# Kernel tuning notes

Measured on AMD Instinct MI355X. Metric: run time of the kernel, lower is better.

Reference implementation:

```python
import jax, jax.numpy as jnp
import numpy as np

LAYERS = 5      # lstm_layers
H = 1           # lstm_hidden_size
IN = 21         # 9 (rot) + 6 (v) + 6 (u)
NEG = 0.1       # LeakyReLU negative slope
EPS = 1e-5      # BatchNorm1d eps


def _lstm_cell(x, h, c, w_ih, w_hh):
    # torch gate order: i, f, g, o ; no biases (lstm_bias=False)
    gates = x @ w_ih.T + h @ w_hh.T              # [k, 4H]
    i, f, g, o = jnp.split(gates, 4, axis=-1)
    i = jax.nn.sigmoid(i)
    f = jax.nn.sigmoid(f)
    g = jnp.tanh(g)
    o = jax.nn.sigmoid(o)
    c_new = f * c + i * g
    h_new = o * jnp.tanh(c_new)
    return h_new, c_new


def _bn_train(z, gamma, beta):
    # BatchNorm1d in training mode: batch stats, biased variance
    m = z.mean(axis=0)
    var = z.var(axis=0)
    return gamma * (z - m) / jnp.sqrt(var + EPS) + beta


def setup_inputs() -> dict:
    key = jax.random.key(0)
    ks = jax.random.split(key, 14)
    k, T = 65536, 32
    s = 0.2  # init scale, roughly torch uniform(-1/sqrt(H)) magnitude
    inp = {
        "r": jax.random.normal(ks[0], (k, T, 9), jnp.float32),
        "v": jax.random.normal(ks[1], (k, T, 6), jnp.float32),
        "u": jax.random.normal(ks[2], (k, T, 6), jnp.float32),
        # LSTM weights: layer 0 sees IN features, layers 1..4 see H
        "w_ih0": jax.random.normal(ks[3], (4 * H, IN), jnp.float32) * s,
        "w_ih_rest": jax.random.normal(ks[4], (LAYERS - 1, 4 * H, H), jnp.float32) * s,
        "w_hh": jax.random.normal(ks[5], (LAYERS, 4 * H, H), jnp.float32) * s,
        # FC head: Linear(H,32,no bias) -> BN -> LReLU -> Linear(32,32) -> BN -> LReLU -> Linear(32,6)
        "W1": jax.random.normal(ks[6], (32, H), jnp.float32) * s,
        "g1": jnp.ones((32,), jnp.float32),
        "b1": jnp.zeros((32,), jnp.float32),
        "W2": jax.random.normal(ks[7], (32, 32), jnp.float32) * s,
        "g2": jnp.ones((32,), jnp.float32),
        "b2": jnp.zeros((32,), jnp.float32),
        "W3": jax.random.normal(ks[8], (6, 32), jnp.float32) * s,
    }
    return inp


def reference(r, v, u, w_ih0, w_ih_rest, w_hh, W1, g1, b1, W2, g2, b2, W3):
    x = jnp.concatenate([r, v, u], axis=-1)          # [k, T, 21]
    k = x.shape[0]
    h0 = jnp.zeros((LAYERS, k, H), x.dtype)
    c0 = jnp.zeros((LAYERS, k, H), x.dtype)
    xs = jnp.swapaxes(x, 0, 1)                       # [T, k, 21]

    def step(carry, xt):
        h, c = carry
        hs, cs = [], []
        layer_in = xt
        for l in range(LAYERS):
            w_ih = w_ih0 if l == 0 else w_ih_rest[l - 1]
            hl, cl = _lstm_cell(layer_in, h[l], c[l], w_ih, w_hh[l])
            hs.append(hl)
            cs.append(cl)
            layer_in = hl
        return (jnp.stack(hs), jnp.stack(cs)), layer_in  # top-layer output

    (hT, cT), outs = jax.lax.scan(step, (h0, c0), xs)    # outs: [T, k, H]

    # fc applied to out[:, 0] -> first timestep of top layer
    y = outs[0]                                          # [k, H]
    y = jax.nn.leaky_relu(_bn_train(y @ W1.T, g1, b1), NEG)
    y = jax.nn.leaky_relu(_bn_train(y @ W2.T, g2, b2), NEG)
    dv = y @ W3.T                                        # [k, 6]
    return dv[:, None], hT, cT
```

## Files before the change

### kernel.cpp

```cpp
#include <hip/hip_runtime.h>
#include <hip/hip_fp16.h>
#include <math.h>

#define T 32
#define NEGS 0.1f
#define EPS 1e-5f
#define NREG 33
#define NH (3 * NREG)


__device__ __forceinline__ float rcp_fast(float x) { return __builtin_amdgcn_rcpf(x); }
__device__ __forceinline__ float sigm(float x) { return rcp_fast(1.0f + __expf(-x)); }
__device__ __forceinline__ float tanh_fast(float x) {
    float t = __expf(2.0f * fabsf(x));
    float r = 1.0f - 2.0f * rcp_fast(t + 1.0f);
    return copysignf(r, x);
}
__device__ __forceinline__ float lrelu(float x) { return x > 0.0f ? x : NEGS * x; }

__device__ __forceinline__ void bn1_ab(const float* __restrict__ W1,
                                       const float* __restrict__ g1,
                                       const float* __restrict__ b1,
                                       float my, float vy, int j,
                                       float& a, float& b, float& tau, int& flip)
{
    float wj = W1[j];
    a = g1[j] * wj * rsqrtf(fmaf(wj * wj, vy, EPS));
    b = b1[j];
    if (a > 0.0f)      { tau = my - b / a; flip = 0; }
    else if (a < 0.0f) { tau = my - b / a; flip = 1; }
    else               { tau = (b > 0.0f ? -__builtin_inff() : __builtin_inff()); flip = 0; }
}

__device__ __forceinline__ void reduce_stats(const double* __restrict__ bSums, int nb, int k,
                                             float* outMy, float* outVy)
{
    const int tid = threadIdx.x;
    double sy = 0.0, sq = 0.0;
    for (int i = tid; i < nb; i += 256) { sy += bSums[2 * i]; sq += bSums[2 * i + 1]; }
#pragma unroll
    for (int off = 32; off; off >>= 1) {
        sy += __shfl_down(sy, off);
        sq += __shfl_down(sq, off);
    }
    __shared__ double dS[4], dQ[4];
    const int wid = tid >> 6, lane = tid & 63;
    if (lane == 0) { dS[wid] = sy; dQ[wid] = sq; }
    __syncthreads();
    if (tid == 0) {
        double tS = dS[0] + dS[1] + dS[2] + dS[3];
        double tQ = dQ[0] + dQ[1] + dQ[2] + dQ[3];
        float my = (float)(tS / k);
        *outMy = my;
        *outVy = (float)(tQ / k) - my * my;
    }
    __syncthreads();
}

__global__ __launch_bounds__(256)
void gates_kernel(const float* __restrict__ r, const float* __restrict__ v,
                  const float* __restrict__ u, const float* __restrict__ wih0,
                  ushort4* __restrict__ xg, int k)
{
    __shared__ float inS[4 * 1344];
    __shared__ ushort4 gbuf[8 * 33];
    const int tid = threadIdx.x;
    const int w = tid >> 6, lane = tid & 63;
    const int s0 = blockIdx.x * 8;

    float wi0[4][21];
#pragma unroll
    for (int g = 0; g < 4; ++g)
#pragma unroll
        for (int j = 0; j < 21; ++j) wi0[g][j] = wih0[g * 21 + j];

    {
        const int sw = s0 + 2 * w;
        const float4* rG = (const float4*)(r + (size_t)sw * 288);
        const float4* vG = (const float4*)(v + (size_t)sw * 192);
        const float4* uG = (const float4*)(u + (size_t)sw * 192);
        float4* wS = ((float4*)inS) + w * 336;
#pragma unroll
        for (int it = 0; it < 6; ++it) {
            int i = lane + it * 64;
            if (i < 336) {
                float4 val = (i < 144) ? rG[i] : (i < 240 ? vG[i - 144] : uG[i - 240]);
                wS[i] = val;
            }
        }
    }
    const int sl = (lane >> 5), t = lane & 31;
    const float* base = inS + w * 1344;
    float x[21];
#pragma unroll
    for (int j = 0; j < 9; ++j) x[j] = base[sl * 288 + t * 9 + j];
#pragma unroll
    for (int j = 0; j < 6; ++j) x[9 + j] = base[576 + sl * 192 + t * 6 + j];
#pragma unroll
    for (int j = 0; j < 6; ++j) x[15 + j] = base[960 + sl * 192 + t * 6 + j];

    float acc[4];
#pragma unroll
    for (int g = 0; g < 4; ++g) {
        float a = 0.f;
#pragma unroll
        for (int j = 0; j < 21; ++j) a = fmaf(wi0[g][j], x[j], a);
        acc[g] = a;
    }
    ushort4 pk;
    pk.x = __half_as_ushort(__float2half(acc[0]));
    pk.y = __half_as_ushort(__float2half(acc[1]));
    pk.z = __half_as_ushort(__float2half(acc[2]));
    pk.w = __half_as_ushort(__float2half(acc[3]));

    const int sblk = 2 * w + sl;
    gbuf[sblk * 33 + t] = pk;
    __syncthreads();

    const int tS = tid >> 3, sS = tid & 7;
    xg[(size_t)tS * k + s0 + sS] = gbuf[sS * 33 + tS];
}

__global__ __launch_bounds__(256, 1)
void recur_kernel(const ushort4* __restrict__ xg, const float* __restrict__ wihr,
                  const float* __restrict__ whhp, float* __restrict__ out,
                  double* __restrict__ bSums, float* __restrict__ wsy, int k)
{
    const int s = blockIdx.x * 256 + threadIdx.x;

    float wir[4][4];
#pragma unroll
    for (int l = 0; l < 4; ++l)
#pragma unroll
        for (int g = 0; g < 4; ++g) wir[l][g] = wihr[l * 4 + g];
    float whh[5][4];
#pragma unroll
    for (int l = 0; l < 5; ++l)
#pragma unroll
        for (int g = 0; g < 4; ++g) whh[l][g] = whhp[l * 4 + g];

    ushort4 gbuf[T];
#pragma unroll
    for (int t = 0; t < T; ++t) gbuf[t] = xg[(size_t)t * k + s];

    float h[5] = {0.f, 0.f, 0.f, 0.f, 0.f};
    float c[5] = {0.f, 0.f, 0.f, 0.f, 0.f};
    float y0 = 0.f;

#pragma unroll
    for (int t = 0; t < T; ++t) {
        const ushort4 G = gbuf[t];
        float a0 = fmaf(whh[0][0], h[0], __half2float(__ushort_as_half(G.x)));
        float a1 = fmaf(whh[0][1], h[0], __half2float(__ushort_as_half(G.y)));
        float a2 = fmaf(whh[0][2], h[0], __half2float(__ushort_as_half(G.z)));
        float a3 = fmaf(whh[0][3], h[0], __half2float(__ushort_as_half(G.w)));
        {
            float ii = sigm(a0), ff = sigm(a1);
            float gg = tanh_fast(a2), oo = sigm(a3);
            c[0] = ff * c[0] + ii * gg;
            h[0] = oo * tanh_fast(c[0]);
        }
        float xin = h[0];
#pragma unroll
        for (int l = 1; l < 5; ++l) {
            float b0 = fmaf(wir[l - 1][0], xin, whh[l][0] * h[l]);
            float b1 = fmaf(wir[l - 1][1], xin, whh[l][1] * h[l]);
            float b2 = fmaf(wir[l - 1][2], xin, whh[l][2] * h[l]);
            float b3 = fmaf(wir[l - 1][3], xin, whh[l][3] * h[l]);
            float ii = sigm(b0), ff = sigm(b1);
            float gg = tanh_fast(b2), oo = sigm(b3);
            c[l] = ff * c[l] + ii * gg;
            h[l] = oo * tanh_fast(c[l]);
            xin = h[l];
        }
        if (t == 0) y0 = h[4];
    }

#pragma unroll
    for (int l = 0; l < 5; ++l) {
        out[(size_t)6 * k + (size_t)l * k + s] = h[l];
        out[(size_t)11 * k + (size_t)l * k + s] = c[l];
    }
    wsy[s] = y0;

    float ys = y0, yq = y0 * y0;
#pragma unroll
    for (int off = 32; off; off >>= 1) {
        ys += __shfl_down(ys, off);
        yq += __shfl_down(yq, off);
    }
    __shared__ float pS[4], pQ[4];
    const int wid = threadIdx.x >> 6, lane = threadIdx.x & 63;
    if (lane == 0) { pS[wid] = ys; pQ[wid] = yq; }
    __syncthreads();
    if (threadIdx.x == 0) {
        bSums[2 * blockIdx.x] = (double)(pS[0] + pS[1] + pS[2] + pS[3]);
        bSums[2 * blockIdx.x + 1] = (double)(pQ[0] + pQ[1] + pQ[2] + pQ[3]);
    }
}

__global__ __launch_bounds__(256, 1)
void lstm_fused(const float* __restrict__ r, const float* __restrict__ v,
                const float* __restrict__ u,
                const float* __restrict__ wih0, const float* __restrict__ wihr,
                const float* __restrict__ whhp,
                float* __restrict__ out, double* __restrict__ bSums,
                float* __restrict__ wsy, int k)
{
    const int s = blockIdx.x * 256 + threadIdx.x;
    float wi0[4][21];
#pragma unroll
    for (int g = 0; g < 4; ++g)
#pragma unroll
        for (int j = 0; j < 21; ++j) wi0[g][j] = wih0[g * 21 + j];
    float wir[4][4];
#pragma unroll
    for (int l = 0; l < 4; ++l)
#pragma unroll
        for (int g = 0; g < 4; ++g) wir[l][g] = wihr[l * 4 + g];
    float whh[5][4];
#pragma unroll
    for (int l = 0; l < 5; ++l)
#pragma unroll
        for (int g = 0; g < 4; ++g) whh[l][g] = whhp[l * 4 + g];

    const float4* r4 = reinterpret_cast<const float4*>(r + (size_t)s * (T * 9));
    const float4* v4 = reinterpret_cast<const float4*>(v + (size_t)s * (T * 6));
    const float4* u4 = reinterpret_cast<const float4*>(u + (size_t)s * (T * 6));

    float h[5] = {0.f, 0.f, 0.f, 0.f, 0.f};
    float c[5] = {0.f, 0.f, 0.f, 0.f, 0.f};
    float y0 = 0.f;

    for (int t0 = 0; t0 < T; t0 += 4) {
        const int cb = t0 >> 2;
        float4 rb[9], vb[6], ub[6];
#pragma unroll
        for (int q = 0; q < 9; ++q) rb[q] = r4[cb * 9 + q];
#pragma unroll
        for (int q = 0; q < 6; ++q) vb[q] = v4[cb * 6 + q];
#pragma unroll
        for (int q = 0; q < 6; ++q) ub[q] = u4[cb * 6 + q];
        float rf[36], vf[24], uf[24];
#pragma unroll
        for (int q = 0; q < 9; ++q) {
            rf[4 * q] = rb[q].x; rf[4 * q + 1] = rb[q].y;
            rf[4 * q + 2] = rb[q].z; rf[4 * q + 3] = rb[q].w;
        }
#pragma unroll
        for (int q = 0; q < 6; ++q) {
            vf[4 * q] = vb[q].x; vf[4 * q + 1] = vb[q].y;
            vf[4 * q + 2] = vb[q].z; vf[4 * q + 3] = vb[q].w;
            uf[4 * q] = ub[q].x; uf[4 * q + 1] = ub[q].y;
            uf[4 * q + 2] = ub[q].z; uf[4 * q + 3] = ub[q].w;
        }
#pragma unroll
        for (int dt = 0; dt < 4; ++dt) {
            float x[21];
#pragma unroll
            for (int j = 0; j < 9; ++j) x[j] = rf[dt * 9 + j];
#pragma unroll
            for (int j = 0; j < 6; ++j) x[9 + j] = vf[dt * 6 + j];
#pragma unroll
            for (int j = 0; j < 6; ++j) x[15 + j] = uf[dt * 6 + j];
            float gt[4];
#pragma unroll
            for (int g = 0; g < 4; ++g) {
                float a = whh[0][g] * h[0];
#pragma unroll
                for (int j = 0; j < 21; ++j) a = fmaf(wi0[g][j], x[j], a);
                gt[g] = a;
            }
            {
                float ii = sigm(gt[0]), ff = sigm(gt[1]);
                float gg = tanh_fast(gt[2]), oo = sigm(gt[3]);
                c[0] = ff * c[0] + ii * gg;
                h[0] = oo * tanh_fast(c[0]);
            }
            float xin = h[0];
#pragma unroll
            for (int l = 1; l < 5; ++l) {
                float b0 = fmaf(wir[l - 1][0], xin, whh[l][0] * h[l]);
                float b1 = fmaf(wir[l - 1][1], xin, whh[l][1] * h[l]);
                float b2 = fmaf(wir[l - 1][2], xin, whh[l][2] * h[l]);
                float b3 = fmaf(wir[l - 1][3], xin, whh[l][3] * h[l]);
                float ii = sigm(b0), ff = sigm(b1);
                float gg = tanh_fast(b2), oo = sigm(b3);
                c[l] = ff * c[l] + ii * gg;
                h[l] = oo * tanh_fast(c[l]);
                xin = h[l];
            }
            if (t0 + dt == 0) y0 = h[4];
        }
    }
#pragma unroll
    for (int l = 0; l < 5; ++l) {
        out[(size_t)6 * k + (size_t)l * k + s] = h[l];
        out[(size_t)11 * k + (size_t)l * k + s] = c[l];
    }
    wsy[s] = y0;
    float ys = y0, yq = y0 * y0;
#pragma unroll
    for (int off = 32; off; off >>= 1) {
        ys += __shfl_down(ys, off);
        yq += __shfl_down(yq, off);
    }
    __shared__ float pS[4], pQ[4];
    const int wid = threadIdx.x >> 6, lane = threadIdx.x & 63;
    if (lane == 0) { pS[wid] = ys; pQ[wid] = yq; }
    __syncthreads();
    if (threadIdx.x == 0) {
        bSums[2 * blockIdx.x] = (double)(pS[0] + pS[1] + pS[2] + pS[3]);
        bSums[2 * blockIdx.x + 1] = (double)(pQ[0] + pQ[1] + pQ[2] + pQ[3]);
    }
}

__global__ __launch_bounds__(256)
void hist_kernel(const float* __restrict__ W1, const float* __restrict__ g1,
                 const float* __restrict__ b1, const double* __restrict__ bSums, int nb,
                 float* __restrict__ bHist, const float* __restrict__ wsy, int k)
{
    __shared__ float sMy, sVy;
    __shared__ float sTau[32];
    __shared__ float sH[NH];
    const int tid = threadIdx.x;
    reduce_stats(bSums, nb, k, &sMy, &sVy);
    if (tid < NH) sH[tid] = 0.f;
    if (tid < 32) {
        float a, b, tau; int flip;
        bn1_ab(W1, g1, b1, sMy, sVy, tid, a, b, tau, flip);
        sTau[tid] = tau;
    }
    __syncthreads();
    const float my = sMy;
    const int stride = gridDim.x * 256;
    for (int s = blockIdx.x * 256 + tid; s < k; s += stride) {
        const float y = wsy[s];
        const float yc = y - my;
        int rgn = 0;
#pragma unroll
        for (int j = 0; j < 32; ++j) rgn += (y > sTau[j]) ? 1 : 0;
        atomicAdd(&sH[rgn], 1.0f);
        atomicAdd(&sH[NREG + rgn], yc);
        atomicAdd(&sH[2 * NREG + rgn], yc * yc);
    }
    __syncthreads();
    if (tid < NH) bHist[blockIdx.x * NH + tid] = sH[tid];
}

__global__ __launch_bounds__(256)
void tables_kernel(const float* __restrict__ W1, const float* __restrict__ g1,
                   const float* __restrict__ b1, const float* __restrict__ W2,
                   const float* __restrict__ g2, const float* __restrict__ b2,
                   const double* __restrict__ bSums, int nb,
                   const float* __restrict__ bHist, int nhb,
                   float* __restrict__ gPQ, int k)
{
    __shared__ float sMy, sVy;
    __shared__ float sA[32], sB[32], sTau[32];
    __shared__ int sRank[32], sFlip[32];
    __shared__ float sS0[NREG], sS1[NREG], sS2[NREG];
    __shared__ float sW2[1024];
    __shared__ float sSumY1[32];
    __shared__ float sM[1024];
    __shared__ float sI2[32], sM2v[32], sB2[32];
    const int tid = threadIdx.x;

    reduce_stats(bSums, nb, k, &sMy, &sVy);
    for (int i = tid; i < 1024; i += 256) sW2[i] = W2[i];
    if (tid < NH) {
        float acc = 0.f;
        for (int bk = 0; bk < nhb; ++bk) acc += bHist[bk * NH + tid];
        if (tid < NREG)           sS0[tid] = acc;
        else if (tid < 2 * NREG)  sS1[tid - NREG] = acc;
        else                      sS2[tid - 2 * NREG] = acc;
    }
    if (tid < 32) {
        float a, b, tau; int flip;
        bn1_ab(W1, g1, b1, sMy, sVy, tid, a, b, tau, flip);
        sA[tid] = a; sB[tid] = b; sTau[tid] = tau; sFlip[tid] = flip;
        sB2[tid] = b2[tid];
    }
    __syncthreads();
    if (tid < 32) {
        int rk = 0;
        float tj = sTau[tid];
#pragma unroll
        for (int l = 0; l < 32; ++l)
            rk += (sTau[l] < tj || (sTau[l] == tj && l < tid)) ? 1 : 0;
        sRank[tid] = rk;
    }
    __syncthreads();
    if (tid < 32) {
        const int rk = sRank[tid], fl = sFlip[tid];
        const float a = sA[tid], b = sB[tid];
        float acc = 0.f;
        for (int rg = 0; rg < NREG; ++rg) {
            float m = (((rk < rg) ? 1 : 0) != fl) ? 1.0f : NEGS;
            acc += m * (a * sS1[rg] + b * sS0[rg]);
        }
        sSumY1[tid] = acc;
    }
    for (int p = tid; p < 1024; p += 256) {
        const int j = p >> 5, l = p & 31;
        const int rj = sRank[j], fj = sFlip[j];
        const int rl = sRank[l], flp = sFlip[l];
        const float aj = sA[j], bj = sB[j], al = sA[l], bl = sB[l];
        const float caa = aj * al, cab = aj * bl + al * bj, cbb = bj * bl;
        float acc = 0.f;
        for (int rg = 0; rg < NREG; ++rg) {
            float mj = (((rj < rg) ? 1 : 0) != fj) ? 1.0f : NEGS;
            float ml = (((rl < rg) ? 1 : 0) != flp) ? 1.0f : NEGS;
            acc += mj * ml * (caa * sS2[rg] + cab * sS1[rg] + cbb * sS0[rg]);
        }
        sM[p] = acc;
    }
    __syncthreads();
    if (tid < 32) {
        const int i = tid;
        float s2 = 0.f, ss2 = 0.f;
#pragma unroll
        for (int j = 0; j < 32; ++j) {
            float wij = sW2[i * 32 + j];
            s2 = fmaf(wij, sSumY1[j], s2);
            float tj = 0.f;
#pragma unroll
            for (int l = 0; l < 32; ++l) tj = fmaf(sW2[i * 32 + l], sM[j * 32 + l], tj);
            ss2 = fmaf(wij, tj, ss2);
        }
        float m2 = s2 / k;
        float v2 = ss2 / k - m2 * m2;
        sM2v[i] = m2;
        sI2[i] = g2[i] * rsqrtf(v2 + EPS);
    }
    __syncthreads();
    for (int idx = tid; idx < NREG * 32; idx += 256) {
        const int rg = idx >> 5, i = idx & 31;
        float Ai = 0.f, Bi = 0.f;
#pragma unroll
        for (int j = 0; j < 32; ++j) {
            float m = (((sRank[j] < rg) ? 1 : 0) != sFlip[j]) ? 1.0f : NEGS;
            float w = sW2[i * 32 + j] * m;
            Ai = fmaf(w, sA[j], Ai);
            Bi = fmaf(w, sB[j], Bi);
        }
        gPQ[idx] = sI2[i] * Ai;
        gPQ[NREG * 32 + idx] = sI2[i] * (Bi - sM2v[i]) + sB2[i];
    }
    if (tid < 32) gPQ[2 * NREG * 32 + tid] = sTau[tid];
    if (tid == 0) gPQ[2 * NREG * 32 + 32] = sMy;
}

__global__ __launch_bounds__(256)
void final_kernel(const float* __restrict__ W3, const float* __restrict__ wsy,
                  const float* __restrict__ gPQ, float* __restrict__ out, int k)
{
    __shared__ float sTau[32], sW3[192], sMy;
    __shared__ float sP[NREG][33], sQ[NREG][33];
    const int tid = threadIdx.x;
    for (int idx = tid; idx < NREG * 32; idx += 256) {
        const int rg = idx >> 5, i = idx & 31;
        sP[rg][i] = gPQ[idx];
        sQ[rg][i] = gPQ[NREG * 32 + idx];
    }
    if (tid < 192) sW3[tid] = W3[tid];
    if (tid < 32) sTau[tid] = gPQ[2 * NREG * 32 + tid];
    if (tid == 0) sMy = gPQ[2 * NREG * 32 + 32];
    __syncthreads();
    const int s = blockIdx.x * 256 + tid;
    const float y = wsy[s];
    const float yc = y - sMy;
    int rgn = 0;
#pragma unroll
    for (int j = 0; j < 32; ++j) rgn += (y > sTau[j]) ? 1 : 0;
    float dv[6] = {0.f, 0.f, 0.f, 0.f, 0.f, 0.f};
#pragma unroll
    for (int i = 0; i < 32; ++i) {
        float y2 = lrelu(fmaf(sP[rgn][i], yc, sQ[rgn][i]));
#pragma unroll
        for (int m = 0; m < 6; ++m) dv[m] = fmaf(sW3[m * 32 + i], y2, dv[m]);
    }
#pragma unroll
    for (int m = 0; m < 6; ++m) out[(size_t)s * 6 + m] = dv[m];
}

extern "C" void kernel_launch(void* const* d_in, const int* in_sizes, int n_in,
                              void* d_out, int out_size, void* d_ws, size_t ws_size,
                              hipStream_t stream)
{
    const float* r    = (const float*)d_in[0];
    const float* v    = (const float*)d_in[1];
    const float* u    = (const float*)d_in[2];
    const float* wih0 = (const float*)d_in[3];
    const float* wihr = (const float*)d_in[4];
    const float* whhp = (const float*)d_in[5];
    const float* W1   = (const float*)d_in[6];
    const float* g1v  = (const float*)d_in[7];
    const float* b1v  = (const float*)d_in[8];
    const float* W2   = (const float*)d_in[9];
    const float* g2v  = (const float*)d_in[10];
    const float* b2v  = (const float*)d_in[11];
    const float* W3   = (const float*)d_in[12];

    const int k = in_sizes[0] / (T * 9);
    const int blocks = k / 256;
    const int HB = 64;
    float* out = (float*)d_out;

    double* bSums = (double*)d_ws;
    float* bHist  = (float*)((char*)d_ws + 4096);
    float* wsy    = (float*)((char*)d_ws + 32768);
    const size_t xg_off = 32768 + (size_t)k * 4;
    const size_t need = xg_off + (size_t)k * T * 8 + 2176 * 4;

    float* gPQ;
    if (ws_size >= need) {
        ushort4* xg = (ushort4*)((char*)d_ws + xg_off);
        gPQ = (float*)((char*)d_ws + xg_off + (size_t)k * T * 8);
        gates_kernel<<<k / 8, 256, 0, stream>>>(r, v, u, wih0, xg, k);
        recur_kernel<<<blocks, 256, 0, stream>>>(xg, wihr, whhp, out, bSums, wsy, k);
    } else {
        gPQ = (float*)((char*)d_ws + xg_off);
        lstm_fused<<<blocks, 256, 0, stream>>>(r, v, u, wih0, wihr, whhp, out, bSums, wsy, k);
    }
    hist_kernel<<<HB, 256, 0, stream>>>(W1, g1v, b1v, bSums, blocks, bHist, wsy, k);
    tables_kernel<<<1, 256, 0, stream>>>(W1, g1v, b1v, W2, g2v, b2v, bSums, blocks,
                                         bHist, HB, gPQ, k);
    final_kernel<<<blocks, 256, 0, stream>>>(W3, wsy, gPQ, out, k);
}
```

Measured before the change: 270.8 us.

## Fuse input-gate projection and recurrence into one kernel via shared-memory staging

The separate gates kernel, which wrote fp16 input-gate preactivations to global memory, and the recurrence kernel that read them back are merged into one kernel. Each 256-thread block has all four waves compute gates for 64 sequences into LDS. A single wave then runs the 32-step recurrence for those sequences reading from LDS. This removes the global round trip of the gate buffer and one launch. The cost is that three of four waves sit idle during the serial recurrence, so far fewer lanes run the long dependent chain at once.

```diff
diff --git a/kernel.cpp b/kernel.cpp
--- a/kernel.cpp
+++ b/kernel.cpp
@@ -58,15 +58,17 @@
 }
 
 __global__ __launch_bounds__(256)
-void gates_kernel(const float* __restrict__ r, const float* __restrict__ v,
-                  const float* __restrict__ u, const float* __restrict__ wih0,
-                  ushort4* __restrict__ xg, int k)
+void lstm_fused_kernel(const float* __restrict__ r, const float* __restrict__ v,
+                       const float* __restrict__ u, const float* __restrict__ wih0,
+                       const float* __restrict__ wihr, const float* __restrict__ whhp,
+                       float* __restrict__ out, double* __restrict__ bSums,
+                       float* __restrict__ wsy, int k)
 {
     __shared__ float inS[4 * 1344];
-    __shared__ ushort4 gbuf[8 * 33];
+    __shared__ ushort4 gbuf[64 * 33];
     const int tid = threadIdx.x;
     const int w = tid >> 6, lane = tid & 63;
-    const int s0 = blockIdx.x * 8;
+    const int sBase = blockIdx.x * 64;
 
     float wi0[4][21];
 #pragma unroll
@@ -74,12 +76,15 @@
 #pragma unroll
         for (int j = 0; j < 21; ++j) wi0[g][j] = wih0[g * 21 + j];
 
-    {
-        const int sw = s0 + 2 * w;
-        const float4* rG = (const float4*)(r + (size_t)sw * 288);
-        const float4* vG = (const float4*)(v + (size_t)sw * 192);
-        const float4* uG = (const float4*)(u + (size_t)sw * 192);
-        float4* wS = ((float4*)inS) + w * 336;
+    const int sl = lane >> 5, t = lane & 31;
+    float4* wS = ((float4*)inS) + w * 336;
+    const float* base = inS + w * 1344;
+
+    for (int c = 0; c < 8; ++c) {
+        const int sw0 = sBase + w * 16 + c * 2;
+        const float4* rG = (const float4*)(r + (size_t)sw0 * 288);
+        const float4* vG = (const float4*)(v + (size_t)sw0 * 192);
+        const float4* uG = (const float4*)(u + (size_t)sw0 * 192);
 #pragma unroll
         for (int it = 0; it < 6; ++it) {
             int i = lane + it * 64;
@@ -88,45 +93,32 @@
                 wS[i] = val;
             }
         }
-    }
-    const int sl = (lane >> 5), t = lane & 31;
-    const float* base = inS + w * 1344;
-    float x[21];
-#pragma unroll
-    for (int j = 0; j < 9; ++j) x[j] = base[sl * 288 + t * 9 + j];
-#pragma unroll
-    for (int j = 0; j < 6; ++j) x[9 + j] = base[576 + sl * 192 + t * 6 + j];
-#pragma unroll
-    for (int j = 0; j < 6; ++j) x[15 + j] = base[960 + sl * 192 + t * 6 + j];
-
-    float acc[4];
-#pragma unroll
-    for (int g = 0; g < 4; ++g) {
-        float a = 0.f;
-#pragma unroll
-        for (int j = 0; j < 21; ++j) a = fmaf(wi0[g][j], x[j], a);
-        acc[g] = a;
-    }
-    ushort4 pk;
-    pk.x = __half_as_ushort(__float2half(acc[0]));
-    pk.y = __half_as_ushort(__float2half(acc[1]));
-    pk.z = __half_as_ushort(__float2half(acc[2]));
-    pk.w = __half_as_ushort(__float2half(acc[3]));
-
-    const int sblk = 2 * w + sl;
-    gbuf[sblk * 33 + t] = pk;
-    __syncthreads();
-
-    const int tS = tid >> 3, sS = tid & 7;
-    xg[(size_t)tS * k + s0 + sS] = gbuf[sS * 33 + tS];
-}
-
-__global__ __launch_bounds__(256, 1)
-void recur_kernel(const ushort4* __restrict__ xg, const float* __restrict__ wihr,
-                  const float* __restrict__ whhp, float* __restrict__ out,
-                  double* __restrict__ bSums, float* __restrict__ wsy, int k)
-{
-    const int s = blockIdx.x * 256 + threadIdx.x;
+        float x[21];
+#pragma unroll
+        for (int j = 0; j < 9; ++j) x[j] = base[sl * 288 + t * 9 + j];
+#pragma unroll
+        for (int j = 0; j < 6; ++j) x[9 + j] = base[576 + sl * 192 + t * 6 + j];
+#pragma unroll
+        for (int j = 0; j < 6; ++j) x[15 + j] = base[960 + sl * 192 + t * 6 + j];
+
+        float acc[4];
+#pragma unroll
+        for (int g = 0; g < 4; ++g) {
+            float a = 0.f;
+#pragma unroll
+            for (int j = 0; j < 21; ++j) a = fmaf(wi0[g][j], x[j], a);
+            acc[g] = a;
+        }
+        ushort4 pk;
+        pk.x = __half_as_ushort(__float2half(acc[0]));
+        pk.y = __half_as_ushort(__float2half(acc[1]));
+        pk.z = __half_as_ushort(__float2half(acc[2]));
+        pk.w = __half_as_ushort(__float2half(acc[3]));
+        const int sb = w * 16 + c * 2 + sl;
+        gbuf[sb * 33 + t] = pk;
+    }
+    __syncthreads();
+    if (tid >= 64) return;
 
     float wir[4][4];
 #pragma unroll
@@ -139,17 +131,14 @@
 #pragma unroll
         for (int g = 0; g < 4; ++g) whh[l][g] = whhp[l * 4 + g];
 
-    ushort4 gbuf[T];
-#pragma unroll
-    for (int t = 0; t < T; ++t) gbuf[t] = xg[(size_t)t * k + s];
-
+    const int s = sBase + lane;
     float h[5] = {0.f, 0.f, 0.f, 0.f, 0.f};
-    float c[5] = {0.f, 0.f, 0.f, 0.f, 0.f};
+    float c5[5] = {0.f, 0.f, 0.f, 0.f, 0.f};
     float y0 = 0.f;
 
 #pragma unroll
-    for (int t = 0; t < T; ++t) {
-        const ushort4 G = gbuf[t];
+    for (int tt = 0; tt < T; ++tt) {
+        const ushort4 G = gbuf[lane * 33 + tt];
         float a0 = fmaf(whh[0][0], h[0], __half2float(__ushort_as_half(G.x)));
         float a1 = fmaf(whh[0][1], h[0], __half2float(__ushort_as_half(G.y)));
         float a2 = fmaf(whh[0][2], h[0], __half2float(__ushort_as_half(G.z)));
@@ -157,8 +146,8 @@
         {
             float ii = sigm(a0), ff = sigm(a1);
             float gg = tanh_fast(a2), oo = sigm(a3);
-            c[0] = ff * c[0] + ii * gg;
-            h[0] = oo * tanh_fast(c[0]);
+            c5[0] = ff * c5[0] + ii * gg;
+            h[0] = oo * tanh_fast(c5[0]);
         }
         float xin = h[0];
 #pragma unroll
@@ -169,17 +158,17 @@
             float b3 = fmaf(wir[l - 1][3], xin, whh[l][3] * h[l]);
             float ii = sigm(b0), ff = sigm(b1);
             float gg = tanh_fast(b2), oo = sigm(b3);
-            c[l] = ff * c[l] + ii * gg;
-            h[l] = oo * tanh_fast(c[l]);
+            c5[l] = ff * c5[l] + ii * gg;
+            h[l] = oo * tanh_fast(c5[l]);
             xin = h[l];
         }
-        if (t == 0) y0 = h[4];
+        if (tt == 0) y0 = h[4];
     }
 
 #pragma unroll
     for (int l = 0; l < 5; ++l) {
         out[(size_t)6 * k + (size_t)l * k + s] = h[l];
-        out[(size_t)11 * k + (size_t)l * k + s] = c[l];
+        out[(size_t)11 * k + (size_t)l * k + s] = c5[l];
     }
     wsy[s] = y0;
 
@@ -189,129 +178,9 @@
         ys += __shfl_down(ys, off);
         yq += __shfl_down(yq, off);
     }
-    __shared__ float pS[4], pQ[4];
-    const int wid = threadIdx.x >> 6, lane = threadIdx.x & 63;
-    if (lane == 0) { pS[wid] = ys; pQ[wid] = yq; }
-    __syncthreads();
-    if (threadIdx.x == 0) {
-        bSums[2 * blockIdx.x] = (double)(pS[0] + pS[1] + pS[2] + pS[3]);
-        bSums[2 * blockIdx.x + 1] = (double)(pQ[0] + pQ[1] + pQ[2] + pQ[3]);
-    }
-}
-
-__global__ __launch_bounds__(256, 1)
-void lstm_fused(const float* __restrict__ r, const float* __restrict__ v,
-                const float* __restrict__ u,
-                const float* __restrict__ wih0, const float* __restrict__ wihr,
-                const float* __restrict__ whhp,
-                float* __restrict__ out, double* __restrict__ bSums,
-                float* __restrict__ wsy, int k)
-{
-    const int s = blockIdx.x * 256 + threadIdx.x;
-    float wi0[4][21];
-#pragma unroll
-    for (int g = 0; g < 4; ++g)
-#pragma unroll
-        for (int j = 0; j < 21; ++j) wi0[g][j] = wih0[g * 21 + j];
-    float wir[4][4];
-#pragma unroll
-    for (int l = 0; l < 4; ++l)
-#pragma unroll
-        for (int g = 0; g < 4; ++g) wir[l][g] = wihr[l * 4 + g];
-    float whh[5][4];
-#pragma unroll
-    for (int l = 0; l < 5; ++l)
-#pragma unroll
-        for (int g = 0; g < 4; ++g) whh[l][g] = whhp[l * 4 + g];
-
-    const float4* r4 = reinterpret_cast<const float4*>(r + (size_t)s * (T * 9));
-    const float4* v4 = reinterpret_cast<const float4*>(v + (size_t)s * (T * 6));
-    const float4* u4 = reinterpret_cast<const float4*>(u + (size_t)s * (T * 6));
-
-    float h[5] = {0.f, 0.f, 0.f, 0.f, 0.f};
-    float c[5] = {0.f, 0.f, 0.f, 0.f, 0.f};
-    float y0 = 0.f;
-
-    for (int t0 = 0; t0 < T; t0 += 4) {
-        const int cb = t0 >> 2;
-        float4 rb[9], vb[6], ub[6];
-#pragma unroll
-        for (int q = 0; q < 9; ++q) rb[q] = r4[cb * 9 + q];
-#pragma unroll
-        for (int q = 0; q < 6; ++q) vb[q] = v4[cb * 6 + q];
-#pragma unroll
-        for (int q = 0; q < 6; ++q) ub[q] = u4[cb * 6 + q];
-        float rf[36], vf[24], uf[24];
-#pragma unroll
-        for (int q = 0; q < 9; ++q) {
-            rf[4 * q] = rb[q].x; rf[4 * q + 1] = rb[q].y;
-            rf[4 * q + 2] = rb[q].z; rf[4 * q + 3] = rb[q].w;
-        }
-#pragma unroll
-        for (int q = 0; q < 6; ++q) {
-            vf[4 * q] = vb[q].x; vf[4 * q + 1] = vb[q].y;
-            vf[4 * q + 2] = vb[q].z; vf[4 * q + 3] = vb[q].w;
-            uf[4 * q] = ub[q].x; uf[4 * q + 1] = ub[q].y;
-            uf[4 * q + 2] = ub[q].z; uf[4 * q + 3] = ub[q].w;
-        }
-#pragma unroll
-        for (int dt = 0; dt < 4; ++dt) {
-            float x[21];
-#pragma unroll
-            for (int j = 0; j < 9; ++j) x[j] = rf[dt * 9 + j];
-#pragma unroll
-            for (int j = 0; j < 6; ++j) x[9 + j] = vf[dt * 6 + j];
-#pragma unroll
-            for (int j = 0; j < 6; ++j) x[15 + j] = uf[dt * 6 + j];
-            float gt[4];
-#pragma unroll
-            for (int g = 0; g < 4; ++g) {
-                float a = whh[0][g] * h[0];
-#pragma unroll
-                for (int j = 0; j < 21; ++j) a = fmaf(wi0[g][j], x[j], a);
-                gt[g] = a;
-            }
-            {
-                float ii = sigm(gt[0]), ff = sigm(gt[1]);
-                float gg = tanh_fast(gt[2]), oo = sigm(gt[3]);
-                c[0] = ff * c[0] + ii * gg;
-                h[0] = oo * tanh_fast(c[0]);
-            }
-            float xin = h[0];
-#pragma unroll
-            for (int l = 1; l < 5; ++l) {
-                float b0 = fmaf(wir[l - 1][0], xin, whh[l][0] * h[l]);
-                float b1 = fmaf(wir[l - 1][1], xin, whh[l][1] * h[l]);
-                float b2 = fmaf(wir[l - 1][2], xin, whh[l][2] * h[l]);
-                float b3 = fmaf(wir[l - 1][3], xin, whh[l][3] * h[l]);
-                float ii = sigm(b0), ff = sigm(b1);
-                float gg = tanh_fast(b2), oo = sigm(b3);
-                c[l] = ff * c[l] + ii * gg;
-                h[l] = oo * tanh_fast(c[l]);
-                xin = h[l];
-            }
-            if (t0 + dt == 0) y0 = h[4];
-        }
-    }
-#pragma unroll
-    for (int l = 0; l < 5; ++l) {
-        out[(size_t)6 * k + (size_t)l * k + s] = h[l];
-        out[(size_t)11 * k + (size_t)l * k + s] = c[l];
-    }
-    wsy[s] = y0;
-    float ys = y0, yq = y0 * y0;
-#pragma unroll
-    for (int off = 32; off; off >>= 1) {
-        ys += __shfl_down(ys, off);
-        yq += __shfl_down(yq, off);
-    }
-    __shared__ float pS[4], pQ[4];
-    const int wid = threadIdx.x >> 6, lane = threadIdx.x & 63;
-    if (lane == 0) { pS[wid] = ys; pQ[wid] = yq; }
-    __syncthreads();
-    if (threadIdx.x == 0) {
-        bSums[2 * blockIdx.x] = (double)(pS[0] + pS[1] + pS[2] + pS[3]);
-        bSums[2 * blockIdx.x + 1] = (double)(pQ[0] + pQ[1] + pQ[2] + pQ[3]);
+    if (lane == 0) {
+        bSums[2 * blockIdx.x] = (double)ys;
+        bSums[2 * blockIdx.x + 1] = (double)yq;
     }
 }
 
@@ -503,28 +372,19 @@
     const float* W3   = (const float*)d_in[12];
 
     const int k = in_sizes[0] / (T * 9);
-    const int blocks = k / 256;
+    const int fblocks = k / 64;
     const int HB = 64;
     float* out = (float*)d_out;
 
     double* bSums = (double*)d_ws;
-    float* bHist  = (float*)((char*)d_ws + 4096);
-    float* wsy    = (float*)((char*)d_ws + 32768);
-    const size_t xg_off = 32768 + (size_t)k * 4;
-    const size_t need = xg_off + (size_t)k * T * 8 + 2176 * 4;
-
-    float* gPQ;
-    if (ws_size >= need) {
-        ushort4* xg = (ushort4*)((char*)d_ws + xg_off);
-        gPQ = (float*)((char*)d_ws + xg_off + (size_t)k * T * 8);
-        gates_kernel<<<k / 8, 256, 0, stream>>>(r, v, u, wih0, xg, k);
-        recur_kernel<<<blocks, 256, 0, stream>>>(xg, wihr, whhp, out, bSums, wsy, k);
-    } else {
-        gPQ = (float*)((char*)d_ws + xg_off);
-        lstm_fused<<<blocks, 256, 0, stream>>>(r, v, u, wih0, wihr, whhp, out, bSums, wsy, k);
-    }
-    hist_kernel<<<HB, 256, 0, stream>>>(W1, g1v, b1v, bSums, blocks, bHist, wsy, k);
-    tables_kernel<<<1, 256, 0, stream>>>(W1, g1v, b1v, W2, g2v, b2v, bSums, blocks,
+    float* bHist  = (float*)((char*)d_ws + 16384);
+    float* wsy    = (float*)((char*)d_ws + 49152);
+    float* gPQ    = (float*)((char*)d_ws + 49152 + (size_t)k * 4);
+
+    lstm_fused_kernel<<<fblocks, 256, 0, stream>>>(r, v, u, wih0, wihr, whhp,
+                                                   out, bSums, wsy, k);
+    hist_kernel<<<HB, 256, 0, stream>>>(W1, g1v, b1v, bSums, fblocks, bHist, wsy, k);
+    tables_kernel<<<1, 256, 0, stream>>>(W1, g1v, b1v, W2, g2v, b2v, bSums, fblocks,
                                          bHist, HB, gPQ, k);
-    final_kernel<<<blocks, 256, 0, stream>>>(W3, wsy, gPQ, out, k);
-}
+    final_kernel<<<k / 256, 256, 0, stream>>>(W3, wsy, gPQ, out, k);
+}
```

Result: slower. 308.3 us (+13.8%).
